# Kernel optimization log

Measured on AMD Instinct MI355X. Metric: run time of the kernel, lower is better.

## Reference

```python
import jax, jax.numpy as jnp
import numpy as np

N_USER = 200000
N_REPO = 100000
N_EDGE = 1500000
D = 128       # input feature dim for both node types
H = 128       # hidden_channels
O = 128       # out_channels


def _sage(x_src, x_dst, src_idx, dst_idx, n_dst, Wl, bl, Wr):
    # PyG SAGEConv: mean-aggregate source features per destination,
    # then lin_l(aggr) + lin_r(x_dst). lin_l has bias, lin_r does not.
    msg = x_src[src_idx]                                   # [E, d_src] gather
    s = jax.ops.segment_sum(msg, dst_idx, num_segments=n_dst)
    cnt = jax.ops.segment_sum(jnp.ones((src_idx.shape[0],), x_src.dtype),
                              dst_idx, num_segments=n_dst)
    mean = s / jnp.maximum(cnt, 1.0)[:, None]
    return mean @ Wl + bl + x_dst @ Wr


def setup_inputs() -> dict:
    key = jax.random.key(0)
    ks = jax.random.split(key, 16)
    s = 1.0 / np.sqrt(D)
    inp = {
        "x_user": jax.random.normal(ks[0], (N_USER, D), jnp.float32),
        "x_repo": jax.random.normal(ks[1], (N_REPO, D), jnp.float32),
        # row 0: user indices, row 1: repo indices
        "edge_stars": jnp.stack([
            jax.random.randint(ks[2], (N_EDGE,), 0, N_USER),
            jax.random.randint(ks[3], (N_EDGE,), 0, N_REPO),
        ]).astype(jnp.int64),
        # layer 1, edge type (user, stars, repo)
        "Wl1s": jax.random.uniform(ks[4], (D, H), jnp.float32, -s, s),
        "bl1s": jnp.zeros((H,), jnp.float32),
        "Wr1s": jax.random.uniform(ks[5], (D, H), jnp.float32, -s, s),
        # layer 1, edge type (repo, rev_stars, user)
        "Wl1r": jax.random.uniform(ks[6], (D, H), jnp.float32, -s, s),
        "bl1r": jnp.zeros((H,), jnp.float32),
        "Wr1r": jax.random.uniform(ks[7], (D, H), jnp.float32, -s, s),
        # layer 2, edge type (user, stars, repo)
        "Wl2s": jax.random.uniform(ks[8], (H, O), jnp.float32, -s, s),
        "bl2s": jnp.zeros((O,), jnp.float32),
        "Wr2s": jax.random.uniform(ks[9], (H, O), jnp.float32, -s, s),
        # layer 2, edge type (repo, rev_stars, user)
        "Wl2r": jax.random.uniform(ks[10], (H, O), jnp.float32, -s, s),
        "bl2r": jnp.zeros((O,), jnp.float32),
        "Wr2r": jax.random.uniform(ks[11], (H, O), jnp.float32, -s, s),
    }
    return inp


def reference(x_user, x_repo, edge_stars,
              Wl1s, bl1s, Wr1s, Wl1r, bl1r, Wr1r,
              Wl2s, bl2s, Wr2s, Wl2r, bl2r, Wr2r):
    u_idx, r_idx = edge_stars[0], edge_stars[1]
    # layer 1: stars (user->repo) updates repo; rev_stars (repo->user) updates user
    repo_h = jax.nn.relu(_sage(x_user, x_repo, u_idx, r_idx, N_REPO, Wl1s, bl1s, Wr1s))
    user_h = jax.nn.relu(_sage(x_repo, x_user, r_idx, u_idx, N_USER, Wl1r, bl1r, Wr1r))
    # layer 2
    repo_out = _sage(user_h, repo_h, u_idx, r_idx, N_REPO, Wl2s, bl2s, Wr2s)
    user_out = _sage(repo_h, user_h, r_idx, u_idx, N_USER, Wl2r, bl2r, Wr2r)
    return user_out, repo_out
```

## Files before the change

### kernel.cpp

```cpp
#include <hip/hip_runtime.h>
#include <stdint.h>

#define NUSER 200000
#define NREPO 100000
#define NEDGE 1500000

#define RB 98
#define UB 196
#define RCAP 17500
#define UCAP 9000

typedef unsigned short u16;
typedef unsigned int u32;
typedef __bf16 bf16x8 __attribute__((ext_vector_type(8)));
typedef float f32x4 __attribute__((ext_vector_type(4)));

#define OFF_RECR 0UL
#define OFF_RECU 6860000UL
#define OFF_B0   0UL
#define OFF_B1   51200000UL
#define OFF_B2   76800000UL
#define OFF_B3   128000000UL
#define OFF_COLR 153600000UL
#define OFF_COLU 159600000UL
#define OFF_POSR 165600000UL
#define OFF_POSU 166000000UL
#define OFF_WT   166800000UL
#define OFF_CUR  167062144UL
#define WS_NEEDED 167064544UL

__device__ __forceinline__ float bflo(u32 p) { return __uint_as_float(p << 16); }
__device__ __forceinline__ float bfhi(u32 p) { return __uint_as_float(p & 0xffff0000u); }
__device__ __forceinline__ u16 f2bf(float f) {
    u32 u = __float_as_uint(f);
    return (u16)((u + 0x7fffu + ((u >> 16) & 1u)) >> 16);
}
__device__ __forceinline__ bf16x8 as_bf16x8(uint4 u) {
    union { uint4 a; bf16x8 b; } x; x.a = u; return x.b;
}

__global__ void sentinel_kernel(float* out) { out[threadIdx.x] = 1234.5f; }

__global__ void zero_i32_kernel(int4* __restrict__ p, int n4) {
    int i = blockIdx.x * blockDim.x + threadIdx.x;
    if (i < n4) p[i] = make_int4(0, 0, 0, 0);
}

__global__ void cvt_bf16_kernel(const float4* __restrict__ in, uint2* __restrict__ out, int n4) {
    int i = blockIdx.x * blockDim.x + threadIdx.x;
    if (i < n4) {
        float4 v = in[i];
        uint2 o;
        o.x = (u32)f2bf(v.x) | ((u32)f2bf(v.y) << 16);
        o.y = (u32)f2bf(v.z) | ((u32)f2bf(v.w) << 16);
        out[i] = o;
    }
}

__global__ void wprep_kernel(const float* __restrict__ Wl, const float* __restrict__ Wr,
                             u16* __restrict__ Wt) {
    int idx = blockIdx.x * blockDim.x + threadIdx.x;
    int n = idx >> 8, k = idx & 255;
    float v = (k < 128) ? Wl[k * 128 + n] : Wr[(k - 128) * 128 + n];
    Wt[idx] = f2bf(v);
}

__device__ __forceinline__ bool detect_is64(const u32* e) {
    __shared__ int any_odd;
    int t = threadIdx.x;
    if (t == 0) any_odd = 0;
    __syncthreads();
    u32 acc = 0;
#pragma unroll
    for (int r = 0; r < 4; ++r) acc |= e[2 * (256 * r + t) + 1];
    if (acc != 0) any_odd = 1;
    __syncthreads();
    return !any_odd;
}

__global__ __launch_bounds__(256)
void passA_bin(const u32* __restrict__ e, u32* __restrict__ rec_r, u32* __restrict__ rec_u,
               int* __restrict__ gcur_r, int* __restrict__ gcur_u) {
    __shared__ int cntR[RB], cntU[UB], baseR[RB], baseU[UB];
    bool is64 = detect_is64(e);
    int t = threadIdx.x;
    for (int i = t; i < RB; i += 256) cntR[i] = 0;
    for (int i = t; i < UB; i += 256) cntU[i] = 0;
    __syncthreads();
    int base = blockIdx.x * 4096;
    int us[16], rs[16];
#pragma unroll
    for (int j = 0; j < 16; ++j) {
        int i = base + j * 256 + t;
        int u = -1, r = -1;
        if (i < NEDGE) {
            u = is64 ? (int)e[2 * i] : (int)e[i];
            r = is64 ? (int)e[2 * (NEDGE + i)] : (int)e[NEDGE + i];
        }
        us[j] = u; rs[j] = r;
        if (u >= 0) { atomicAdd(&cntR[r >> 10], 1); atomicAdd(&cntU[u >> 10], 1); }
    }
    __syncthreads();
    for (int i = t; i < RB; i += 256) baseR[i] = cntR[i] ? atomicAdd(&gcur_r[i], cntR[i]) : 0;
    for (int i = t; i < UB; i += 256) baseU[i] = cntU[i] ? atomicAdd(&gcur_u[i], cntU[i]) : 0;
    __syncthreads();
    for (int i = t; i < RB; i += 256) cntR[i] = 0;
    for (int i = t; i < UB; i += 256) cntU[i] = 0;
    __syncthreads();
#pragma unroll
    for (int j = 0; j < 16; ++j) {
        int u = us[j], r = rs[j];
        if (u >= 0) {
            int br = r >> 10, bu = u >> 10;
            int rk = baseR[br] + atomicAdd(&cntR[br], 1);
            if (rk < RCAP) rec_r[br * RCAP + rk] = ((u32)u << 10) | (u32)(r & 1023);
            int ku = baseU[bu] + atomicAdd(&cntU[bu], 1);
            if (ku < UCAP) rec_u[bu * UCAP + ku] = ((u32)r << 10) | (u32)(u & 1023);
        }
    }
}

__global__ void bucket_scan(const int* __restrict__ gcur_r, const int* __restrict__ gcur_u,
                            int* __restrict__ cb_r, int* __restrict__ cb_u) {
    __shared__ int s0[256], s1[256];
    int t = threadIdx.x;
    s0[t] = (t < RB) ? min(gcur_r[t], RCAP) : 0;
    __syncthreads();
    int* src = s0; int* dst = s1;
    for (int off = 1; off < 256; off <<= 1) {
        int x = src[t]; if (t >= off) x += src[t - off];
        dst[t] = x; __syncthreads();
        int* tmp = src; src = dst; dst = tmp;
    }
    if (t < RB) cb_r[t] = (t == 0) ? 0 : src[t - 1];
    __syncthreads();
    src[t] = 0; __syncthreads();
    s0[t] = (t < UB) ? min(gcur_u[t], UCAP) : 0;
    __syncthreads();
    src = s0; dst = s1;
    for (int off = 1; off < 256; off <<= 1) {
        int x = src[t]; if (t >= off) x += src[t - off];
        dst[t] = x; __syncthreads();
        int* tmp = src; src = dst; dst = tmp;
    }
    if (t < UB) cb_u[t] = (t == 0) ? 0 : src[t - 1];
}

__global__ __launch_bounds__(256)
void passB_build(const u32* __restrict__ rec_r, const u32* __restrict__ rec_u,
                 const int* __restrict__ gcur_r, const int* __restrict__ gcur_u,
                 const int* __restrict__ cb_r, const int* __restrict__ cb_u,
                 int* __restrict__ col_r, int* __restrict__ col_u,
                 int* __restrict__ pos_r, int* __restrict__ pos_u) {
    __shared__ int cnt[1024];
    __shared__ int excl[1024];
    __shared__ int sc0[256], sc1[256];
    int b = blockIdx.x;
    const u32* rec; int count, colbase, dstbase, ndst; int* col; int* pos;
    if (b < RB) {
        rec = rec_r + (size_t)b * RCAP; count = min(gcur_r[b], RCAP); colbase = cb_r[b];
        dstbase = b << 10; ndst = min(1024, NREPO - dstbase); col = col_r; pos = pos_r;
    } else {
        int c = b - RB;
        rec = rec_u + (size_t)c * UCAP; count = min(gcur_u[c], UCAP); colbase = cb_u[c];
        dstbase = c << 10; ndst = min(1024, NUSER - dstbase); col = col_u; pos = pos_u;
    }
    int t = threadIdx.x;
    for (int i = t; i < 1024; i += 256) cnt[i] = 0;
    __syncthreads();
    for (int i = t; i < count; i += 256) atomicAdd(&cnt[rec[i] & 1023], 1);
    __syncthreads();
    int c0 = cnt[t * 4], c1 = cnt[t * 4 + 1], c2 = cnt[t * 4 + 2], c3 = cnt[t * 4 + 3];
    int tsum = c0 + c1 + c2 + c3;
    sc0[t] = tsum; __syncthreads();
    int* src = sc0; int* dst = sc1;
    for (int off = 1; off < 256; off <<= 1) {
        int x = src[t]; if (t >= off) x += src[t - off];
        dst[t] = x; __syncthreads();
        int* tmp = src; src = dst; dst = tmp;
    }
    int exclT = src[t] - tsum;
    int e0 = exclT, e1 = e0 + c0, e2 = e1 + c1, e3 = e2 + c2;
    excl[t * 4] = e0; excl[t * 4 + 1] = e1; excl[t * 4 + 2] = e2; excl[t * 4 + 3] = e3;
    {
        int i = t * 4;
        if (i < ndst)     pos[dstbase + i]     = colbase + e1;
        if (i + 1 < ndst) pos[dstbase + i + 1] = colbase + e2;
        if (i + 2 < ndst) pos[dstbase + i + 2] = colbase + e3;
        if (i + 3 < ndst) pos[dstbase + i + 3] = colbase + e3 + c3;
    }
    __syncthreads();
    for (int i = t; i < 1024; i += 256) cnt[i] = 0;
    __syncthreads();
    for (int i = t; i < count; i += 256) {
        u32 rc = rec[i];
        int dl = rc & 1023;
        int rk = atomicAdd(&cnt[dl], 1);
        col[colbase + excl[dl] + rk] = (int)(rc >> 10);
    }
}

__global__ __launch_bounds__(256)
void gather_mean_kernel(const u16* __restrict__ feat, const int* __restrict__ col,
                        const int* __restrict__ pos, u16* __restrict__ outm, int ndst) {
    int gw = (blockIdx.x * blockDim.x + threadIdx.x) >> 6;
    int lane = threadIdx.x & 63;
    int g = lane >> 4, s = lane & 15;
    if (gw >= ndst) return;
    int start = (gw == 0) ? 0 : pos[gw - 1];
    int end = pos[gw];
    int deg = end - start;
    if (deg <= 0) {
        if (g == 0) {
            uint4 z = make_uint4(0, 0, 0, 0);
            *(uint4*)(outm + (size_t)gw * 128 + s * 8) = z;
        }
        return;
    }
    int mdeg = min(deg, 64);
    int cv = col[start + min(lane, mdeg - 1)];

    float acc[8];
#pragma unroll
    for (int j = 0; j < 8; ++j) acc[j] = 0.f;

    for (int e0 = 0; e0 < mdeg; e0 += 8) {
        int i0 = e0 + g, i1 = e0 + 4 + g;
        int idx0 = __shfl(cv, min(i0, mdeg - 1), 64);
        int idx1 = __shfl(cv, min(i1, mdeg - 1), 64);
        uint4 v0 = *(const uint4*)(feat + (size_t)idx0 * 128 + s * 8);
        uint4 v1 = *(const uint4*)(feat + (size_t)idx1 * 128 + s * 8);
        u32 k0 = (i0 < deg) ? 0xffffffffu : 0u;
        u32 k1 = (i1 < deg) ? 0xffffffffu : 0u;
        v0.x &= k0; v0.y &= k0; v0.z &= k0; v0.w &= k0;
        v1.x &= k1; v1.y &= k1; v1.z &= k1; v1.w &= k1;
        acc[0] += bflo(v0.x) + bflo(v1.x);
        acc[1] += bfhi(v0.x) + bfhi(v1.x);
        acc[2] += bflo(v0.y) + bflo(v1.y);
        acc[3] += bfhi(v0.y) + bfhi(v1.y);
        acc[4] += bflo(v0.z) + bflo(v1.z);
        acc[5] += bfhi(v0.z) + bfhi(v1.z);
        acc[6] += bflo(v0.w) + bflo(v1.w);
        acc[7] += bfhi(v0.w) + bfhi(v1.w);
    }
    for (int e = 64 + g; e < deg; e += 4) {
        int idx = col[start + e];
        uint4 v = *(const uint4*)(feat + (size_t)idx * 128 + s * 8);
        acc[0] += bflo(v.x); acc[1] += bfhi(v.x);
        acc[2] += bflo(v.y); acc[3] += bfhi(v.y);
        acc[4] += bflo(v.z); acc[5] += bfhi(v.z);
        acc[6] += bflo(v.w); acc[7] += bfhi(v.w);
    }

#pragma unroll
    for (int j = 0; j < 8; ++j) {
        acc[j] += __shfl_xor(acc[j], 16, 64);
        acc[j] += __shfl_xor(acc[j], 32, 64);
    }

    if (g == 0) {
        float inv = 1.0f / (float)deg;
        uint4 o;
        o.x = (u32)f2bf(acc[0] * inv) | ((u32)f2bf(acc[1] * inv) << 16);
        o.y = (u32)f2bf(acc[2] * inv) | ((u32)f2bf(acc[3] * inv) << 16);
        o.z = (u32)f2bf(acc[4] * inv) | ((u32)f2bf(acc[5] * inv) << 16);
        o.w = (u32)f2bf(acc[6] * inv) | ((u32)f2bf(acc[7] * inv) << 16);
        *(uint4*)(outm + (size_t)gw * 128 + s * 8) = o;
    }
}

__global__ __launch_bounds__(256)
void transform_mfma(const u16* __restrict__ A, const u16* __restrict__ X,
                    const u16* __restrict__ Wt, const float* __restrict__ bias,
                    u16* __restrict__ out_bf, float* __restrict__ out_f32,
                    int N, int do_relu) {
    __shared__ __align__(16) u16 sA[64][264];
    int tid = threadIdx.x;
    int w = tid >> 6, lane = tid & 63;
    int q = lane >> 4, n = lane & 15;
    int nb = w * 32;

    bf16x8 bfrag[2][8];
#pragma unroll
    for (int nt = 0; nt < 2; ++nt)
#pragma unroll
        for (int ks = 0; ks < 8; ++ks)
            bfrag[nt][ks] = as_bf16x8(*(const uint4*)(Wt + (size_t)(nb + nt * 16 + n) * 256 + ks * 32 + q * 8));
    float bv[2] = { bias[nb + n], bias[nb + 16 + n] };

    int base = blockIdx.x * 64;
    {
        int r = tid >> 2, c = tid & 3;
        int node = base + r;
        uint4 z = make_uint4(0, 0, 0, 0);
        uint4 va[4], vx[4];
        if (node < N) {
            const uint4* pa = (const uint4*)(A + (size_t)node * 128 + c * 32);
            const uint4* px = (const uint4*)(X + (size_t)node * 128 + c * 32);
#pragma unroll
            for (int j = 0; j < 4; ++j) { va[j] = pa[j]; vx[j] = px[j]; }
        } else {
#pragma unroll
            for (int j = 0; j < 4; ++j) { va[j] = z; vx[j] = z; }
        }
#pragma unroll
        for (int j = 0; j < 4; ++j) {
            *(uint4*)&sA[r][c * 32 + j * 8] = va[j];
            *(uint4*)&sA[r][128 + c * 32 + j * 8] = vx[j];
        }
    }
    __syncthreads();

    f32x4 zz = { 0.f, 0.f, 0.f, 0.f };
    f32x4 acc[4][2];
#pragma unroll
    for (int mt = 0; mt < 4; ++mt) { acc[mt][0] = zz; acc[mt][1] = zz; }

#pragma unroll
    for (int ks = 0; ks < 8; ++ks)
#pragma unroll
        for (int mt = 0; mt < 4; ++mt) {
            bf16x8 af = *(const bf16x8*)&sA[mt * 16 + n][ks * 32 + q * 8];
            acc[mt][0] = __builtin_amdgcn_mfma_f32_16x16x32_bf16(af, bfrag[0][ks], acc[mt][0], 0, 0, 0);
            acc[mt][1] = __builtin_amdgcn_mfma_f32_16x16x32_bf16(af, bfrag[1][ks], acc[mt][1], 0, 0, 0);
        }

#pragma unroll
    for (int mt = 0; mt < 4; ++mt) {
        int row0 = base + mt * 16 + q * 4;
#pragma unroll
        for (int nt = 0; nt < 2; ++nt) {
            int colg = nb + nt * 16 + n;
#pragma unroll
            for (int r = 0; r < 4; ++r) {
                int row = row0 + r;
                if (row < N) {
                    float v = acc[mt][nt][r] + bv[nt];
                    if (do_relu) v = fmaxf(v, 0.f);
                    if (out_bf) out_bf[(size_t)row * 128 + colg] = f2bf(v);
                    else        out_f32[(size_t)row * 128 + colg] = v;
                }
            }
        }
    }
}

extern "C" void kernel_launch(void* const* d_in, const int* in_sizes, int n_in,
                              void* d_out, int out_size, void* d_ws, size_t ws_size,
                              hipStream_t stream) {
    const float* x_user = (const float*)d_in[0];
    const float* x_repo = (const float*)d_in[1];
    const u32* edges = (const u32*)d_in[2];
    const float* Wl1s = (const float*)d_in[3], *bl1s = (const float*)d_in[4], *Wr1s = (const float*)d_in[5];
    const float* Wl1r = (const float*)d_in[6], *bl1r = (const float*)d_in[7], *Wr1r = (const float*)d_in[8];
    const float* Wl2s = (const float*)d_in[9], *bl2s = (const float*)d_in[10], *Wr2s = (const float*)d_in[11];
    const float* Wl2r = (const float*)d_in[12], *bl2r = (const float*)d_in[13], *Wr2r = (const float*)d_in[14];

    float* out_user = (float*)d_out;
    float* out_repo = (float*)d_out + (size_t)NUSER * 128;

    if (ws_size < WS_NEEDED) {
        hipLaunchKernelGGL(sentinel_kernel, dim3(1), dim3(256), 0, stream, out_user);
        return;
    }

    char* ws = (char*)d_ws;
    u32* rec_r = (u32*)(ws + OFF_RECR);
    u32* rec_u = (u32*)(ws + OFF_RECU);
    u16* B0 = (u16*)(ws + OFF_B0);
    u16* B1 = (u16*)(ws + OFF_B1);
    u16* B2 = (u16*)(ws + OFF_B2);
    u16* B3 = (u16*)(ws + OFF_B3);
    int* col_r = (int*)(ws + OFF_COLR);
    int* col_u = (int*)(ws + OFF_COLU);
    int* pos_r = (int*)(ws + OFF_POSR);
    int* pos_u = (int*)(ws + OFF_POSU);
    u16* wt1s = (u16*)(ws + OFF_WT);
    u16* wt1r = wt1s + 32768;
    u16* wt2s = wt1r + 32768;
    u16* wt2r = wt2s + 32768;
    int* gcur_r = (int*)(ws + OFF_CUR);
    int* gcur_u = (int*)(ws + OFF_CUR + 400);
    int* cb_r   = (int*)(ws + OFF_CUR + 1200);
    int* cb_u   = (int*)(ws + OFF_CUR + 1600);

    hipLaunchKernelGGL(zero_i32_kernel, dim3(1), dim3(256), 0, stream, (int4*)gcur_r, 300 / 4);
    hipLaunchKernelGGL(passA_bin, dim3(367), dim3(256), 0, stream, edges, rec_r, rec_u, gcur_r, gcur_u);
    hipLaunchKernelGGL(bucket_scan, dim3(1), dim3(256), 0, stream, gcur_r, gcur_u, cb_r, cb_u);
    hipLaunchKernelGGL(passB_build, dim3(RB + UB), dim3(256), 0, stream,
                       rec_r, rec_u, gcur_r, gcur_u, cb_r, cb_u, col_r, col_u, pos_r, pos_u);

    hipLaunchKernelGGL(wprep_kernel, dim3(128), dim3(256), 0, stream, Wl1s, Wr1s, wt1s);
    hipLaunchKernelGGL(wprep_kernel, dim3(128), dim3(256), 0, stream, Wl1r, Wr1r, wt1r);
    hipLaunchKernelGGL(wprep_kernel, dim3(128), dim3(256), 0, stream, Wl2s, Wr2s, wt2s);
    hipLaunchKernelGGL(wprep_kernel, dim3(128), dim3(256), 0, stream, Wl2r, Wr2r, wt2r);
    hipLaunchKernelGGL(cvt_bf16_kernel, dim3(25000), dim3(256), 0, stream,
                       (const float4*)x_user, (uint2*)B2, NUSER * 128 / 4);
    hipLaunchKernelGGL(cvt_bf16_kernel, dim3(12500), dim3(256), 0, stream,
                       (const float4*)x_repo, (uint2*)B3, NREPO * 128 / 4);

    hipLaunchKernelGGL(gather_mean_kernel, dim3(25000), dim3(256), 0, stream, B2, col_r, pos_r, B1, NREPO);
    hipLaunchKernelGGL(gather_mean_kernel, dim3(50000), dim3(256), 0, stream, B3, col_u, pos_u, B0, NUSER);
    hipLaunchKernelGGL(transform_mfma, dim3((NREPO + 63) / 64), dim3(256), 0, stream,
                       B1, B3, wt1s, bl1s, B1, (float*)nullptr, NREPO, 1);
    hipLaunchKernelGGL(transform_mfma, dim3((NUSER + 63) / 64), dim3(256), 0, stream,
                       B0, B2, wt1r, bl1r, B0, (float*)nullptr, NUSER, 1);

    hipLaunchKernelGGL(gather_mean_kernel, dim3(25000), dim3(256), 0, stream, B0, col_r, pos_r, B3, NREPO);
    hipLaunchKernelGGL(gather_mean_kernel, dim3(50000), dim3(256), 0, stream, B1, col_u, pos_u, B2, NUSER);
    hipLaunchKernelGGL(transform_mfma, dim3((NREPO + 63) / 64), dim3(256), 0, stream,
                       B3, B1, wt2s, bl2s, (u16*)nullptr, out_repo, NREPO, 0);
    hipLaunchKernelGGL(transform_mfma, dim3((NUSER + 63) / 64), dim3(256), 0, stream,
                       B2, B0, wt2r, bl2r, (u16*)nullptr, out_user, NUSER, 0);
}
```

Before: 737.8 us.

## Fuse mean-aggregation gather with MFMA transform into one kernel per layer

Replaces the separate gather_mean and transform_mfma kernels with one fused kernel per layer. Each block gathers the neighbour means for its 64 nodes straight into shared memory and then runs the MFMA transform, so the intermediate mean buffer is never written to or re-read from global memory. Both edge directions are merged into a single launch, and the gather loop gains a short-degree fast path and an unroll of 16 neighbours per iteration. In exchange, each wave now processes 16 nodes in sequence instead of one wave per node, which reduces the parallelism available to hide gather latency.

```diff
diff --git a/kernel.cpp b/kernel.cpp
--- a/kernel.cpp
+++ b/kernel.cpp
@@ -201,128 +201,159 @@
 }
 
 __global__ __launch_bounds__(256)
-void gather_mean_kernel(const u16* __restrict__ feat, const int* __restrict__ col,
-                        const int* __restrict__ pos, u16* __restrict__ outm, int ndst) {
-    int gw = (blockIdx.x * blockDim.x + threadIdx.x) >> 6;
-    int lane = threadIdx.x & 63;
-    int g = lane >> 4, s = lane & 15;
-    if (gw >= ndst) return;
-    int start = (gw == 0) ? 0 : pos[gw - 1];
-    int end = pos[gw];
-    int deg = end - start;
-    if (deg <= 0) {
-        if (g == 0) {
-            uint4 z = make_uint4(0, 0, 0, 0);
-            *(uint4*)(outm + (size_t)gw * 128 + s * 8) = z;
-        }
-        return;
-    }
-    int mdeg = min(deg, 64);
-    int cv = col[start + min(lane, mdeg - 1)];
-
-    float acc[8];
-#pragma unroll
-    for (int j = 0; j < 8; ++j) acc[j] = 0.f;
-
-    for (int e0 = 0; e0 < mdeg; e0 += 8) {
-        int i0 = e0 + g, i1 = e0 + 4 + g;
-        int idx0 = __shfl(cv, min(i0, mdeg - 1), 64);
-        int idx1 = __shfl(cv, min(i1, mdeg - 1), 64);
-        uint4 v0 = *(const uint4*)(feat + (size_t)idx0 * 128 + s * 8);
-        uint4 v1 = *(const uint4*)(feat + (size_t)idx1 * 128 + s * 8);
-        u32 k0 = (i0 < deg) ? 0xffffffffu : 0u;
-        u32 k1 = (i1 < deg) ? 0xffffffffu : 0u;
-        v0.x &= k0; v0.y &= k0; v0.z &= k0; v0.w &= k0;
-        v1.x &= k1; v1.y &= k1; v1.z &= k1; v1.w &= k1;
-        acc[0] += bflo(v0.x) + bflo(v1.x);
-        acc[1] += bfhi(v0.x) + bfhi(v1.x);
-        acc[2] += bflo(v0.y) + bflo(v1.y);
-        acc[3] += bfhi(v0.y) + bfhi(v1.y);
-        acc[4] += bflo(v0.z) + bflo(v1.z);
-        acc[5] += bfhi(v0.z) + bfhi(v1.z);
-        acc[6] += bflo(v0.w) + bflo(v1.w);
-        acc[7] += bfhi(v0.w) + bfhi(v1.w);
-    }
-    for (int e = 64 + g; e < deg; e += 4) {
-        int idx = col[start + e];
-        uint4 v = *(const uint4*)(feat + (size_t)idx * 128 + s * 8);
-        acc[0] += bflo(v.x); acc[1] += bfhi(v.x);
-        acc[2] += bflo(v.y); acc[3] += bfhi(v.y);
-        acc[4] += bflo(v.z); acc[5] += bfhi(v.z);
-        acc[6] += bflo(v.w); acc[7] += bfhi(v.w);
-    }
-
-#pragma unroll
-    for (int j = 0; j < 8; ++j) {
-        acc[j] += __shfl_xor(acc[j], 16, 64);
-        acc[j] += __shfl_xor(acc[j], 32, 64);
-    }
-
-    if (g == 0) {
-        float inv = 1.0f / (float)deg;
-        uint4 o;
-        o.x = (u32)f2bf(acc[0] * inv) | ((u32)f2bf(acc[1] * inv) << 16);
-        o.y = (u32)f2bf(acc[2] * inv) | ((u32)f2bf(acc[3] * inv) << 16);
-        o.z = (u32)f2bf(acc[4] * inv) | ((u32)f2bf(acc[5] * inv) << 16);
-        o.w = (u32)f2bf(acc[6] * inv) | ((u32)f2bf(acc[7] * inv) << 16);
-        *(uint4*)(outm + (size_t)gw * 128 + s * 8) = o;
-    }
-}
-
-__global__ __launch_bounds__(256)
-void transform_mfma(const u16* __restrict__ A, const u16* __restrict__ X,
-                    const u16* __restrict__ Wt, const float* __restrict__ bias,
-                    u16* __restrict__ out_bf, float* __restrict__ out_f32,
-                    int N, int do_relu) {
+void fused_sage_layer(
+    const u16* __restrict__ featA, const int* __restrict__ colA, const int* __restrict__ posA,
+    const u16* __restrict__ xA, const u16* __restrict__ WtA, const float* __restrict__ biasA,
+    u16* __restrict__ obfA, float* __restrict__ of32A, int NA, int nblkA,
+    const u16* __restrict__ featB, const int* __restrict__ colB, const int* __restrict__ posB,
+    const u16* __restrict__ xB, const u16* __restrict__ WtB, const float* __restrict__ biasB,
+    u16* __restrict__ obfB, float* __restrict__ of32B, int NB,
+    int do_relu)
+{
     __shared__ __align__(16) u16 sA[64][264];
+    const u16* feat; const int* col; const int* pos; const u16* xd; const u16* Wt;
+    const float* bias; u16* out_bf; float* out_f32; int N, base;
+    if ((int)blockIdx.x < nblkA) {
+        feat = featA; col = colA; pos = posA; xd = xA; Wt = WtA; bias = biasA;
+        out_bf = obfA; out_f32 = of32A; N = NA; base = blockIdx.x * 64;
+    } else {
+        feat = featB; col = colB; pos = posB; xd = xB; Wt = WtB; bias = biasB;
+        out_bf = obfB; out_f32 = of32B; N = NB; base = (blockIdx.x - nblkA) * 64;
+    }
+
     int tid = threadIdx.x;
     int w = tid >> 6, lane = tid & 63;
-    int q = lane >> 4, n = lane & 15;
-    int nb = w * 32;
-
-    bf16x8 bfrag[2][8];
-#pragma unroll
-    for (int nt = 0; nt < 2; ++nt)
-#pragma unroll
-        for (int ks = 0; ks < 8; ++ks)
-            bfrag[nt][ks] = as_bf16x8(*(const uint4*)(Wt + (size_t)(nb + nt * 16 + n) * 256 + ks * 32 + q * 8));
-    float bv[2] = { bias[nb + n], bias[nb + 16 + n] };
-
-    int base = blockIdx.x * 64;
+    int g = lane >> 4, s = lane & 15;
+
     {
         int r = tid >> 2, c = tid & 3;
         int node = base + r;
         uint4 z = make_uint4(0, 0, 0, 0);
-        uint4 va[4], vx[4];
+        uint4 vx[4];
         if (node < N) {
-            const uint4* pa = (const uint4*)(A + (size_t)node * 128 + c * 32);
-            const uint4* px = (const uint4*)(X + (size_t)node * 128 + c * 32);
-#pragma unroll
-            for (int j = 0; j < 4; ++j) { va[j] = pa[j]; vx[j] = px[j]; }
+            const uint4* px = (const uint4*)(xd + (size_t)node * 128 + c * 32);
+#pragma unroll
+            for (int j = 0; j < 4; ++j) vx[j] = px[j];
         } else {
 #pragma unroll
-            for (int j = 0; j < 4; ++j) { va[j] = z; vx[j] = z; }
-        }
-#pragma unroll
-        for (int j = 0; j < 4; ++j) {
-            *(uint4*)&sA[r][c * 32 + j * 8] = va[j];
+            for (int j = 0; j < 4; ++j) vx[j] = z;
+        }
+#pragma unroll
+        for (int j = 0; j < 4; ++j)
             *(uint4*)&sA[r][128 + c * 32 + j * 8] = vx[j];
-        }
-    }
+    }
+
+    for (int j = 0; j < 16; ++j) {
+        int r = w * 16 + j;
+        int node = base + r;
+        float acc[8];
+#pragma unroll
+        for (int k = 0; k < 8; ++k) acc[k] = 0.f;
+        int deg = 0;
+        if (node < N) {
+            int start = (node == 0) ? 0 : pos[node - 1];
+            int end = pos[node];
+            deg = end - start;
+            if (deg > 0) {
+                int mdeg = min(deg, 64);
+                int cv = col[start + min(lane, mdeg - 1)];
+                if (mdeg <= 8) {
+                    int i0 = g, i1 = 4 + g;
+                    int idx0 = __shfl(cv, min(i0, mdeg - 1), 64);
+                    int idx1 = __shfl(cv, min(i1, mdeg - 1), 64);
+                    uint4 v0 = *(const uint4*)(feat + (size_t)idx0 * 128 + s * 8);
+                    uint4 v1 = *(const uint4*)(feat + (size_t)idx1 * 128 + s * 8);
+                    u32 k0 = (i0 < deg) ? 0xffffffffu : 0u;
+                    u32 k1 = (i1 < deg) ? 0xffffffffu : 0u;
+                    v0.x &= k0; v0.y &= k0; v0.z &= k0; v0.w &= k0;
+                    v1.x &= k1; v1.y &= k1; v1.z &= k1; v1.w &= k1;
+                    acc[0] += bflo(v0.x) + bflo(v1.x);
+                    acc[1] += bfhi(v0.x) + bfhi(v1.x);
+                    acc[2] += bflo(v0.y) + bflo(v1.y);
+                    acc[3] += bfhi(v0.y) + bfhi(v1.y);
+                    acc[4] += bflo(v0.z) + bflo(v1.z);
+                    acc[5] += bfhi(v0.z) + bfhi(v1.z);
+                    acc[6] += bflo(v0.w) + bflo(v1.w);
+                    acc[7] += bfhi(v0.w) + bfhi(v1.w);
+                } else {
+                    for (int e0 = 0; e0 < mdeg; e0 += 16) {
+                        int i0 = e0 + g, i1 = e0 + 4 + g, i2 = e0 + 8 + g, i3 = e0 + 12 + g;
+                        int idx0 = __shfl(cv, min(i0, mdeg - 1), 64);
+                        int idx1 = __shfl(cv, min(i1, mdeg - 1), 64);
+                        int idx2 = __shfl(cv, min(i2, mdeg - 1), 64);
+                        int idx3 = __shfl(cv, min(i3, mdeg - 1), 64);
+                        uint4 v0 = *(const uint4*)(feat + (size_t)idx0 * 128 + s * 8);
+                        uint4 v1 = *(const uint4*)(feat + (size_t)idx1 * 128 + s * 8);
+                        uint4 v2 = *(const uint4*)(feat + (size_t)idx2 * 128 + s * 8);
+                        uint4 v3 = *(const uint4*)(feat + (size_t)idx3 * 128 + s * 8);
+                        u32 k0 = (i0 < deg) ? 0xffffffffu : 0u;
+                        u32 k1 = (i1 < deg) ? 0xffffffffu : 0u;
+                        u32 k2 = (i2 < deg) ? 0xffffffffu : 0u;
+                        u32 k3 = (i3 < deg) ? 0xffffffffu : 0u;
+                        v0.x &= k0; v0.y &= k0; v0.z &= k0; v0.w &= k0;
+                        v1.x &= k1; v1.y &= k1; v1.z &= k1; v1.w &= k1;
+                        v2.x &= k2; v2.y &= k2; v2.z &= k2; v2.w &= k2;
+                        v3.x &= k3; v3.y &= k3; v3.z &= k3; v3.w &= k3;
+                        acc[0] += (bflo(v0.x) + bflo(v1.x)) + (bflo(v2.x) + bflo(v3.x));
+                        acc[1] += (bfhi(v0.x) + bfhi(v1.x)) + (bfhi(v2.x) + bfhi(v3.x));
+                        acc[2] += (bflo(v0.y) + bflo(v1.y)) + (bflo(v2.y) + bflo(v3.y));
+                        acc[3] += (bfhi(v0.y) + bfhi(v1.y)) + (bfhi(v2.y) + bfhi(v3.y));
+                        acc[4] += (bflo(v0.z) + bflo(v1.z)) + (bflo(v2.z) + bflo(v3.z));
+                        acc[5] += (bfhi(v0.z) + bfhi(v1.z)) + (bfhi(v2.z) + bfhi(v3.z));
+                        acc[6] += (bflo(v0.w) + bflo(v1.w)) + (bflo(v2.w) + bflo(v3.w));
+                        acc[7] += (bfhi(v0.w) + bfhi(v1.w)) + (bfhi(v2.w) + bfhi(v3.w));
+                    }
+                }
+                for (int e = 64 + g; e < deg; e += 4) {
+                    int idx = col[start + e];
+                    uint4 v = *(const uint4*)(feat + (size_t)idx * 128 + s * 8);
+                    acc[0] += bflo(v.x); acc[1] += bfhi(v.x);
+                    acc[2] += bflo(v.y); acc[3] += bfhi(v.y);
+                    acc[4] += bflo(v.z); acc[5] += bfhi(v.z);
+                    acc[6] += bflo(v.w); acc[7] += bfhi(v.w);
+                }
+#pragma unroll
+                for (int k = 0; k < 8; ++k) {
+                    acc[k] += __shfl_xor(acc[k], 16, 64);
+                    acc[k] += __shfl_xor(acc[k], 32, 64);
+                }
+            }
+        }
+        if (g == 0) {
+            float inv = (deg > 0) ? 1.0f / (float)deg : 0.f;
+            uint4 o;
+            o.x = (u32)f2bf(acc[0] * inv) | ((u32)f2bf(acc[1] * inv) << 16);
+            o.y = (u32)f2bf(acc[2] * inv) | ((u32)f2bf(acc[3] * inv) << 16);
+            o.z = (u32)f2bf(acc[4] * inv) | ((u32)f2bf(acc[5] * inv) << 16);
+            o.w = (u32)f2bf(acc[6] * inv) | ((u32)f2bf(acc[7] * inv) << 16);
+            *(uint4*)&sA[r][s * 8] = o;
+        }
+    }
+
+    int q = g, n = s;
+    int nb = w * 32;
+    bf16x8 bfrag[2][8];
+#pragma unroll
+    for (int nt = 0; nt < 2; ++nt)
+#pragma unroll
+        for (int ks = 0; ks < 8; ++ks)
+            bfrag[nt][ks] = as_bf16x8(*(const uint4*)(Wt + (size_t)(nb + nt * 16 + n) * 256 + ks * 32 + q * 8));
+    float bv[2] = { bias[nb + n], bias[nb + 16 + n] };
+
     __syncthreads();
 
     f32x4 zz = { 0.f, 0.f, 0.f, 0.f };
-    f32x4 acc[4][2];
-#pragma unroll
-    for (int mt = 0; mt < 4; ++mt) { acc[mt][0] = zz; acc[mt][1] = zz; }
+    f32x4 acc2[4][2];
+#pragma unroll
+    for (int mt = 0; mt < 4; ++mt) { acc2[mt][0] = zz; acc2[mt][1] = zz; }
 
 #pragma unroll
     for (int ks = 0; ks < 8; ++ks)
 #pragma unroll
         for (int mt = 0; mt < 4; ++mt) {
             bf16x8 af = *(const bf16x8*)&sA[mt * 16 + n][ks * 32 + q * 8];
-            acc[mt][0] = __builtin_amdgcn_mfma_f32_16x16x32_bf16(af, bfrag[0][ks], acc[mt][0], 0, 0, 0);
-            acc[mt][1] = __builtin_amdgcn_mfma_f32_16x16x32_bf16(af, bfrag[1][ks], acc[mt][1], 0, 0, 0);
+            acc2[mt][0] = __builtin_amdgcn_mfma_f32_16x16x32_bf16(af, bfrag[0][ks], acc2[mt][0], 0, 0, 0);
+            acc2[mt][1] = __builtin_amdgcn_mfma_f32_16x16x32_bf16(af, bfrag[1][ks], acc2[mt][1], 0, 0, 0);
         }
 
 #pragma unroll
@@ -332,10 +363,10 @@
         for (int nt = 0; nt < 2; ++nt) {
             int colg = nb + nt * 16 + n;
 #pragma unroll
-            for (int r = 0; r < 4; ++r) {
-                int row = row0 + r;
+            for (int rr = 0; rr < 4; ++rr) {
+                int row = row0 + rr;
                 if (row < N) {
-                    float v = acc[mt][nt][r] + bv[nt];
+                    float v = acc2[mt][nt][rr] + bv[nt];
                     if (do_relu) v = fmaxf(v, 0.f);
                     if (out_bf) out_bf[(size_t)row * 128 + colg] = f2bf(v);
                     else        out_f32[(size_t)row * 128 + colg] = v;
@@ -384,6 +415,9 @@
     int* cb_r   = (int*)(ws + OFF_CUR + 1200);
     int* cb_u   = (int*)(ws + OFF_CUR + 1600);
 
+    const int nblkR = (NREPO + 63) / 64;
+    const int nblkU = (NUSER + 63) / 64;
+
     hipLaunchKernelGGL(zero_i32_kernel, dim3(1), dim3(256), 0, stream, (int4*)gcur_r, 300 / 4);
     hipLaunchKernelGGL(passA_bin, dim3(367), dim3(256), 0, stream, edges, rec_r, rec_u, gcur_r, gcur_u);
     hipLaunchKernelGGL(bucket_scan, dim3(1), dim3(256), 0, stream, gcur_r, gcur_u, cb_r, cb_u);
@@ -399,17 +433,13 @@
     hipLaunchKernelGGL(cvt_bf16_kernel, dim3(12500), dim3(256), 0, stream,
                        (const float4*)x_repo, (uint2*)B3, NREPO * 128 / 4);
 
-    hipLaunchKernelGGL(gather_mean_kernel, dim3(25000), dim3(256), 0, stream, B2, col_r, pos_r, B1, NREPO);
-    hipLaunchKernelGGL(gather_mean_kernel, dim3(50000), dim3(256), 0, stream, B3, col_u, pos_u, B0, NUSER);
-    hipLaunchKernelGGL(transform_mfma, dim3((NREPO + 63) / 64), dim3(256), 0, stream,
-                       B1, B3, wt1s, bl1s, B1, (float*)nullptr, NREPO, 1);
-    hipLaunchKernelGGL(transform_mfma, dim3((NUSER + 63) / 64), dim3(256), 0, stream,
-                       B0, B2, wt1r, bl1r, B0, (float*)nullptr, NUSER, 1);
-
-    hipLaunchKernelGGL(gather_mean_kernel, dim3(25000), dim3(256), 0, stream, B0, col_r, pos_r, B3, NREPO);
-    hipLaunchKernelGGL(gather_mean_kernel, dim3(50000), dim3(256), 0, stream, B1, col_u, pos_u, B2, NUSER);
-    hipLaunchKernelGGL(transform_mfma, dim3((NREPO + 63) / 64), dim3(256), 0, stream,
-                       B3, B1, wt2s, bl2s, (u16*)nullptr, out_repo, NREPO, 0);
-    hipLaunchKernelGGL(transform_mfma, dim3((NUSER + 63) / 64), dim3(256), 0, stream,
-                       B2, B0, wt2r, bl2r, (u16*)nullptr, out_user, NUSER, 0);
-}
+    hipLaunchKernelGGL(fused_sage_layer, dim3(nblkR + nblkU), dim3(256), 0, stream,
+                       B2, col_r, pos_r, B3, wt1s, bl1s, B1, (float*)nullptr, NREPO, nblkR,
+                       B3, col_u, pos_u, B2, wt1r, bl1r, B0, (float*)nullptr, NUSER,
+                       1);
+
+    hipLaunchKernelGGL(fused_sage_layer, dim3(nblkR + nblkU), dim3(256), 0, stream,
+                       B0, col_r, pos_r, B1, wt2s, bl2s, (u16*)nullptr, out_repo, NREPO, nblkR,
+                       B1, col_u, pos_u, B0, wt2r, bl2r, (u16*)nullptr, out_user, NUSER,
+                       0);
+}
```

Result: slower. 769.1 us (+4.2%).

## Merge paired launches and process two destinations per wave in gather

Applied to the files above, without the earlier changes.

Merges the four weight-prep launches into one and the two bf16 conversions into one. It also fuses the repo and user gather-mean and transform launches of each layer into single grids that branch per wave or block. The gather now assigns two destination nodes per 64-lane wave, 32 lanes each, with four outstanding row loads per iteration instead of two. This cuts launch count and tail effects and lets both edge directions overlap on the device. The cost is lanes left idle on low-degree nodes and extra branching to select which operand set a wave uses.

```diff
diff --git a/kernel.cpp b/kernel.cpp
--- a/kernel.cpp
+++ b/kernel.cpp
@@ -46,23 +46,31 @@
     if (i < n4) p[i] = make_int4(0, 0, 0, 0);
 }
 
-__global__ void cvt_bf16_kernel(const float4* __restrict__ in, uint2* __restrict__ out, int n4) {
+__global__ void cvt_bf16_both(const float4* __restrict__ inA, uint2* __restrict__ outA, int n4A,
+                              const float4* __restrict__ inB, uint2* __restrict__ outB, int n4B) {
     int i = blockIdx.x * blockDim.x + threadIdx.x;
-    if (i < n4) {
-        float4 v = in[i];
-        uint2 o;
-        o.x = (u32)f2bf(v.x) | ((u32)f2bf(v.y) << 16);
-        o.y = (u32)f2bf(v.z) | ((u32)f2bf(v.w) << 16);
-        out[i] = o;
-    }
-}
-
-__global__ void wprep_kernel(const float* __restrict__ Wl, const float* __restrict__ Wr,
-                             u16* __restrict__ Wt) {
-    int idx = blockIdx.x * blockDim.x + threadIdx.x;
+    const float4* in; uint2* out; int idx;
+    if (i < n4A) { in = inA; out = outA; idx = i; }
+    else { in = inB; out = outB; idx = i - n4A; if (idx >= n4B) return; }
+    float4 v = in[idx];
+    uint2 o;
+    o.x = (u32)f2bf(v.x) | ((u32)f2bf(v.y) << 16);
+    o.y = (u32)f2bf(v.z) | ((u32)f2bf(v.w) << 16);
+    out[idx] = o;
+}
+
+__global__ void wprep4_kernel(const float* __restrict__ Wl0, const float* __restrict__ Wr0,
+                              const float* __restrict__ Wl1, const float* __restrict__ Wr1,
+                              const float* __restrict__ Wl2, const float* __restrict__ Wr2,
+                              const float* __restrict__ Wl3, const float* __restrict__ Wr3,
+                              u16* __restrict__ Wt) {
+    int which = blockIdx.x >> 7;
+    const float* Wl = (which == 0) ? Wl0 : (which == 1) ? Wl1 : (which == 2) ? Wl2 : Wl3;
+    const float* Wr = (which == 0) ? Wr0 : (which == 1) ? Wr1 : (which == 2) ? Wr2 : Wr3;
+    int idx = (blockIdx.x & 127) * 256 + threadIdx.x;
     int n = idx >> 8, k = idx & 255;
     float v = (k < 128) ? Wl[k * 128 + n] : Wr[(k - 128) * 128 + n];
-    Wt[idx] = f2bf(v);
+    Wt[which * 32768 + idx] = f2bf(v);
 }
 
 __device__ __forceinline__ bool detect_is64(const u32* e) {
@@ -201,80 +209,102 @@
 }
 
 __global__ __launch_bounds__(256)
-void gather_mean_kernel(const u16* __restrict__ feat, const int* __restrict__ col,
-                        const int* __restrict__ pos, u16* __restrict__ outm, int ndst) {
+void gather_mean2(const u16* __restrict__ featA, const int* __restrict__ colA,
+                  const int* __restrict__ posA, u16* __restrict__ outA, int ndstA, int nwaveA,
+                  const u16* __restrict__ featB, const int* __restrict__ colB,
+                  const int* __restrict__ posB, u16* __restrict__ outB, int ndstB) {
     int gw = (blockIdx.x * blockDim.x + threadIdx.x) >> 6;
+    const u16* feat; const int* col; const int* pos; u16* outm; int ndst, dbase;
+    if (gw < nwaveA) {
+        feat = featA; col = colA; pos = posA; outm = outA; ndst = ndstA; dbase = gw * 2;
+    } else {
+        feat = featB; col = colB; pos = posB; outm = outB; ndst = ndstB; dbase = (gw - nwaveA) * 2;
+    }
     int lane = threadIdx.x & 63;
-    int g = lane >> 4, s = lane & 15;
-    if (gw >= ndst) return;
-    int start = (gw == 0) ? 0 : pos[gw - 1];
-    int end = pos[gw];
+    int h = lane >> 5, l5 = lane & 31, g2 = l5 >> 4, s = l5 & 15;
+    int d = dbase + h;
+    if (d >= ndst) return;
+
+    int start = (d == 0) ? 0 : pos[d - 1];
+    int end = pos[d];
     int deg = end - start;
-    if (deg <= 0) {
-        if (g == 0) {
-            uint4 z = make_uint4(0, 0, 0, 0);
-            *(uint4*)(outm + (size_t)gw * 128 + s * 8) = z;
-        }
-        return;
-    }
-    int mdeg = min(deg, 64);
-    int cv = col[start + min(lane, mdeg - 1)];
 
     float acc[8];
 #pragma unroll
-    for (int j = 0; j < 8; ++j) acc[j] = 0.f;
-
-    for (int e0 = 0; e0 < mdeg; e0 += 8) {
-        int i0 = e0 + g, i1 = e0 + 4 + g;
-        int idx0 = __shfl(cv, min(i0, mdeg - 1), 64);
-        int idx1 = __shfl(cv, min(i1, mdeg - 1), 64);
-        uint4 v0 = *(const uint4*)(feat + (size_t)idx0 * 128 + s * 8);
-        uint4 v1 = *(const uint4*)(feat + (size_t)idx1 * 128 + s * 8);
-        u32 k0 = (i0 < deg) ? 0xffffffffu : 0u;
-        u32 k1 = (i1 < deg) ? 0xffffffffu : 0u;
-        v0.x &= k0; v0.y &= k0; v0.z &= k0; v0.w &= k0;
-        v1.x &= k1; v1.y &= k1; v1.z &= k1; v1.w &= k1;
-        acc[0] += bflo(v0.x) + bflo(v1.x);
-        acc[1] += bfhi(v0.x) + bfhi(v1.x);
-        acc[2] += bflo(v0.y) + bflo(v1.y);
-        acc[3] += bfhi(v0.y) + bfhi(v1.y);
-        acc[4] += bflo(v0.z) + bflo(v1.z);
-        acc[5] += bfhi(v0.z) + bfhi(v1.z);
-        acc[6] += bflo(v0.w) + bflo(v1.w);
-        acc[7] += bfhi(v0.w) + bfhi(v1.w);
-    }
-    for (int e = 64 + g; e < deg; e += 4) {
-        int idx = col[start + e];
-        uint4 v = *(const uint4*)(feat + (size_t)idx * 128 + s * 8);
-        acc[0] += bflo(v.x); acc[1] += bfhi(v.x);
-        acc[2] += bflo(v.y); acc[3] += bfhi(v.y);
-        acc[4] += bflo(v.z); acc[5] += bfhi(v.z);
-        acc[6] += bflo(v.w); acc[7] += bfhi(v.w);
-    }
-
-#pragma unroll
-    for (int j = 0; j < 8; ++j) {
-        acc[j] += __shfl_xor(acc[j], 16, 64);
-        acc[j] += __shfl_xor(acc[j], 32, 64);
-    }
-
-    if (g == 0) {
-        float inv = 1.0f / (float)deg;
+    for (int k = 0; k < 8; ++k) acc[k] = 0.f;
+
+    if (deg > 0) {
+        int mdeg = min(deg, 32);
+        int cv = col[start + min(l5, mdeg - 1)];
+        int hb = h * 32;
+        for (int e0 = 0; e0 < mdeg; e0 += 8) {
+            int i0 = e0 + g2, i1 = e0 + 2 + g2, i2 = e0 + 4 + g2, i3 = e0 + 6 + g2;
+            int idx0 = __shfl(cv, hb + min(i0, mdeg - 1), 64);
+            int idx1 = __shfl(cv, hb + min(i1, mdeg - 1), 64);
+            int idx2 = __shfl(cv, hb + min(i2, mdeg - 1), 64);
+            int idx3 = __shfl(cv, hb + min(i3, mdeg - 1), 64);
+            uint4 v0 = *(const uint4*)(feat + (size_t)idx0 * 128 + s * 8);
+            uint4 v1 = *(const uint4*)(feat + (size_t)idx1 * 128 + s * 8);
+            uint4 v2 = *(const uint4*)(feat + (size_t)idx2 * 128 + s * 8);
+            uint4 v3 = *(const uint4*)(feat + (size_t)idx3 * 128 + s * 8);
+            u32 k0 = (i0 < deg) ? 0xffffffffu : 0u;
+            u32 k1 = (i1 < deg) ? 0xffffffffu : 0u;
+            u32 k2 = (i2 < deg) ? 0xffffffffu : 0u;
+            u32 k3 = (i3 < deg) ? 0xffffffffu : 0u;
+            v0.x &= k0; v0.y &= k0; v0.z &= k0; v0.w &= k0;
+            v1.x &= k1; v1.y &= k1; v1.z &= k1; v1.w &= k1;
+            v2.x &= k2; v2.y &= k2; v2.z &= k2; v2.w &= k2;
+            v3.x &= k3; v3.y &= k3; v3.z &= k3; v3.w &= k3;
+            acc[0] += (bflo(v0.x) + bflo(v1.x)) + (bflo(v2.x) + bflo(v3.x));
+            acc[1] += (bfhi(v0.x) + bfhi(v1.x)) + (bfhi(v2.x) + bfhi(v3.x));
+            acc[2] += (bflo(v0.y) + bflo(v1.y)) + (bflo(v2.y) + bflo(v3.y));
+            acc[3] += (bfhi(v0.y) + bfhi(v1.y)) + (bfhi(v2.y) + bfhi(v3.y));
+            acc[4] += (bflo(v0.z) + bflo(v1.z)) + (bflo(v2.z) + bflo(v3.z));
+            acc[5] += (bfhi(v0.z) + bfhi(v1.z)) + (bfhi(v2.z) + bfhi(v3.z));
+            acc[6] += (bflo(v0.w) + bflo(v1.w)) + (bflo(v2.w) + bflo(v3.w));
+            acc[7] += (bfhi(v0.w) + bfhi(v1.w)) + (bfhi(v2.w) + bfhi(v3.w));
+        }
+        for (int e = 32 + g2; e < deg; e += 2) {
+            int idx = col[start + e];
+            uint4 v = *(const uint4*)(feat + (size_t)idx * 128 + s * 8);
+            acc[0] += bflo(v.x); acc[1] += bfhi(v.x);
+            acc[2] += bflo(v.y); acc[3] += bfhi(v.y);
+            acc[4] += bflo(v.z); acc[5] += bfhi(v.z);
+            acc[6] += bflo(v.w); acc[7] += bfhi(v.w);
+        }
+#pragma unroll
+        for (int k = 0; k < 8; ++k) acc[k] += __shfl_xor(acc[k], 16, 64);
+    }
+
+    if (g2 == 0) {
+        float inv = (deg > 0) ? 1.0f / (float)deg : 0.f;
         uint4 o;
         o.x = (u32)f2bf(acc[0] * inv) | ((u32)f2bf(acc[1] * inv) << 16);
         o.y = (u32)f2bf(acc[2] * inv) | ((u32)f2bf(acc[3] * inv) << 16);
         o.z = (u32)f2bf(acc[4] * inv) | ((u32)f2bf(acc[5] * inv) << 16);
         o.w = (u32)f2bf(acc[6] * inv) | ((u32)f2bf(acc[7] * inv) << 16);
-        *(uint4*)(outm + (size_t)gw * 128 + s * 8) = o;
+        *(uint4*)(outm + (size_t)d * 128 + s * 8) = o;
     }
 }
 
 __global__ __launch_bounds__(256)
-void transform_mfma(const u16* __restrict__ A, const u16* __restrict__ X,
-                    const u16* __restrict__ Wt, const float* __restrict__ bias,
-                    u16* __restrict__ out_bf, float* __restrict__ out_f32,
-                    int N, int do_relu) {
+void transform_both(const u16* __restrict__ A_A, const u16* __restrict__ X_A,
+                    const u16* __restrict__ Wt_A, const float* __restrict__ b_A,
+                    u16* __restrict__ obf_A, float* __restrict__ of32_A, int N_A, int nblkA,
+                    const u16* __restrict__ A_B, const u16* __restrict__ X_B,
+                    const u16* __restrict__ Wt_B, const float* __restrict__ b_B,
+                    u16* __restrict__ obf_B, float* __restrict__ of32_B, int N_B,
+                    int do_relu) {
     __shared__ __align__(16) u16 sA[64][264];
+    const u16* A; const u16* X; const u16* Wt; const float* bias;
+    u16* out_bf; float* out_f32; int N, base;
+    if ((int)blockIdx.x < nblkA) {
+        A = A_A; X = X_A; Wt = Wt_A; bias = b_A; out_bf = obf_A; out_f32 = of32_A;
+        N = N_A; base = blockIdx.x * 64;
+    } else {
+        A = A_B; X = X_B; Wt = Wt_B; bias = b_B; out_bf = obf_B; out_f32 = of32_B;
+        N = N_B; base = (blockIdx.x - nblkA) * 64;
+    }
     int tid = threadIdx.x;
     int w = tid >> 6, lane = tid & 63;
     int q = lane >> 4, n = lane & 15;
@@ -288,7 +318,6 @@
             bfrag[nt][ks] = as_bf16x8(*(const uint4*)(Wt + (size_t)(nb + nt * 16 + n) * 256 + ks * 32 + q * 8));
     float bv[2] = { bias[nb + n], bias[nb + 16 + n] };
 
-    int base = blockIdx.x * 64;
     {
         int r = tid >> 2, c = tid & 3;
         int node = base + r;
@@ -384,32 +413,37 @@
     int* cb_r   = (int*)(ws + OFF_CUR + 1200);
     int* cb_u   = (int*)(ws + OFF_CUR + 1600);
 
+    const int nblkR = (NREPO + 63) / 64;
+    const int nblkU = (NUSER + 63) / 64;
+    const int nwaveR = NREPO / 2;
+    const int nwaveU = NUSER / 2;
+    const int gblk = (nwaveR + nwaveU) / 4;
+
     hipLaunchKernelGGL(zero_i32_kernel, dim3(1), dim3(256), 0, stream, (int4*)gcur_r, 300 / 4);
     hipLaunchKernelGGL(passA_bin, dim3(367), dim3(256), 0, stream, edges, rec_r, rec_u, gcur_r, gcur_u);
     hipLaunchKernelGGL(bucket_scan, dim3(1), dim3(256), 0, stream, gcur_r, gcur_u, cb_r, cb_u);
     hipLaunchKernelGGL(passB_build, dim3(RB + UB), dim3(256), 0, stream,
                        rec_r, rec_u, gcur_r, gcur_u, cb_r, cb_u, col_r, col_u, pos_r, pos_u);
 
-    hipLaunchKernelGGL(wprep_kernel, dim3(128), dim3(256), 0, stream, Wl1s, Wr1s, wt1s);
-    hipLaunchKernelGGL(wprep_kernel, dim3(128), dim3(256), 0, stream, Wl1r, Wr1r, wt1r);
-    hipLaunchKernelGGL(wprep_kernel, dim3(128), dim3(256), 0, stream, Wl2s, Wr2s, wt2s);
-    hipLaunchKernelGGL(wprep_kernel, dim3(128), dim3(256), 0, stream, Wl2r, Wr2r, wt2r);
-    hipLaunchKernelGGL(cvt_bf16_kernel, dim3(25000), dim3(256), 0, stream,
-                       (const float4*)x_user, (uint2*)B2, NUSER * 128 / 4);
-    hipLaunchKernelGGL(cvt_bf16_kernel, dim3(12500), dim3(256), 0, stream,
+    hipLaunchKernelGGL(wprep4_kernel, dim3(512), dim3(256), 0, stream,
+                       Wl1s, Wr1s, Wl1r, Wr1r, Wl2s, Wr2s, Wl2r, Wr2r, wt1s);
+    hipLaunchKernelGGL(cvt_bf16_both, dim3(37500), dim3(256), 0, stream,
+                       (const float4*)x_user, (uint2*)B2, NUSER * 128 / 4,
                        (const float4*)x_repo, (uint2*)B3, NREPO * 128 / 4);
 
-    hipLaunchKernelGGL(gather_mean_kernel, dim3(25000), dim3(256), 0, stream, B2, col_r, pos_r, B1, NREPO);
-    hipLaunchKernelGGL(gather_mean_kernel, dim3(50000), dim3(256), 0, stream, B3, col_u, pos_u, B0, NUSER);
-    hipLaunchKernelGGL(transform_mfma, dim3((NREPO + 63) / 64), dim3(256), 0, stream,
-                       B1, B3, wt1s, bl1s, B1, (float*)nullptr, NREPO, 1);
-    hipLaunchKernelGGL(transform_mfma, dim3((NUSER + 63) / 64), dim3(256), 0, stream,
-                       B0, B2, wt1r, bl1r, B0, (float*)nullptr, NUSER, 1);
-
-    hipLaunchKernelGGL(gather_mean_kernel, dim3(25000), dim3(256), 0, stream, B0, col_r, pos_r, B3, NREPO);
-    hipLaunchKernelGGL(gather_mean_kernel, dim3(50000), dim3(256), 0, stream, B1, col_u, pos_u, B2, NUSER);
-    hipLaunchKernelGGL(transform_mfma, dim3((NREPO + 63) / 64), dim3(256), 0, stream,
-                       B3, B1, wt2s, bl2s, (u16*)nullptr, out_repo, NREPO, 0);
-    hipLaunchKernelGGL(transform_mfma, dim3((NUSER + 63) / 64), dim3(256), 0, stream,
-                       B2, B0, wt2r, bl2r, (u16*)nullptr, out_user, NUSER, 0);
-}
+    hipLaunchKernelGGL(gather_mean2, dim3(gblk), dim3(256), 0, stream,
+                       B2, col_r, pos_r, B1, NREPO, nwaveR,
+                       B3, col_u, pos_u, B0, NUSER);
+    hipLaunchKernelGGL(transform_both, dim3(nblkR + nblkU), dim3(256), 0, stream,
+                       B1, B3, wt1s, bl1s, B1, (float*)nullptr, NREPO, nblkR,
+                       B0, B2, wt1r, bl1r, B0, (float*)nullptr, NUSER,
+                       1);
+
+    hipLaunchKernelGGL(gather_mean2, dim3(gblk), dim3(256), 0, stream,
+                       B0, col_r, pos_r, B3, NREPO, nwaveR,
+                       B1, col_u, pos_u, B2, NUSER);
+    hipLaunchKernelGGL(transform_both, dim3(nblkR + nblkU), dim3(256), 0, stream,
+                       B3, B1, wt2s, bl2s, (u16*)nullptr, out_repo, NREPO, nblkR,
+                       B2, B0, wt2r, bl2r, (u16*)nullptr, out_user, NUSER,
+                       0);
+}
```

New measurement: 680.9 us. 7.7% less time.
